# Kernel optimization log

Measured on AMD Instinct MI355X. Metric: run time of the kernel, lower is better.

The kernel has to match this reference:

```python
import jax, jax.numpy as jnp
import numpy as np

B, S, H, E, V, P = 64, 1024, 512, 512, 32000, 40


def setup_inputs() -> dict:
    key = jax.random.key(0)
    ks = jax.random.split(key, 18)
    s = 0.05  # weight scale to keep tanh/sigmoid in active range
    inp = {}
    inp["input_token"] = jax.random.randint(ks[0], (B,), 0, V, dtype=jnp.int32)
    inp["hidden"] = jax.random.normal(ks[1], (1, B, H), jnp.float32)
    inp["cell"] = jax.random.normal(ks[2], (1, B, H), jnp.float32)
    inp["encoder_outputs"] = jax.random.normal(ks[3], (B, S, H), jnp.float32)
    pos_ids = jax.random.randint(ks[4], (B, S), 0, P)
    inp["pos_onehot"] = jax.nn.one_hot(pos_ids, P, dtype=jnp.float32)
    inp["src_mask"] = jnp.zeros((B, S), dtype=bool)  # no PAD (avoids all -inf rows)
    # learned parameters (torch Linear convention: y = x @ W.T + b)
    inp["embed_table"] = jax.random.normal(ks[5], (V, E), jnp.float32) * s
    inp["W_s"] = jax.random.normal(ks[6], (H, H), jnp.float32) * s
    inp["W_h"] = jax.random.normal(ks[7], (H, H), jnp.float32) * s
    inp["V_w"] = jax.random.normal(ks[8], (H,), jnp.float32) * s
    inp["W_p"] = jax.random.normal(ks[9], (P,), jnp.float32) * s
    inp["b_p"] = jax.random.normal(ks[10], (), jnp.float32) * s
    inp["W_ih"] = jax.random.normal(ks[11], (4 * H, E + H), jnp.float32) * s
    inp["W_hh"] = jax.random.normal(ks[12], (4 * H, H), jnp.float32) * s
    inp["b_ih"] = jax.random.normal(ks[13], (4 * H,), jnp.float32) * s
    inp["b_hh"] = jax.random.normal(ks[14], (4 * H,), jnp.float32) * s
    inp["W_out"] = jax.random.normal(ks[15], (V, H), jnp.float32) * s
    inp["b_out"] = jax.random.normal(ks[16], (V,), jnp.float32) * s
    return inp


def reference(input_token, hidden, cell, encoder_outputs, pos_onehot, src_mask,
              embed_table, W_s, W_h, V_w, W_p, b_p,
              W_ih, W_hh, b_ih, b_hh, W_out, b_out):
    # embedding (dropout is identity in eval)
    emb = embed_table[input_token]                                  # (B, E)
    q = hidden[-1]                                                  # (B, H)
    # POS-gated Bahdanau attention
    qs = q @ W_s.T                                                  # (B, H)
    eh = jnp.einsum('bsh,kh->bsk', encoder_outputs, W_h)            # (B, S, H)
    energy = jnp.tanh(qs[:, None, :] + eh)                          # (B, S, H)
    scores = jnp.einsum('bsh,h->bs', energy, V_w)                   # (B, S)
    gate = jax.nn.sigmoid(pos_onehot @ W_p + b_p)                   # (B, S)
    gated = jnp.where(src_mask, jnp.float32(-1e30), scores * gate)
    attn = jax.nn.softmax(gated, axis=-1)                           # (B, S)
    context = jnp.einsum('bs,bsh->bh', attn, encoder_outputs)       # (B, H)
    # single-step, single-layer LSTM (torch gate order: i, f, g, o)
    lstm_in = jnp.concatenate([emb, context], axis=-1)              # (B, E+H)
    gates = lstm_in @ W_ih.T + hidden[0] @ W_hh.T + b_ih + b_hh     # (B, 4H)
    i, f, g, o = jnp.split(gates, 4, axis=-1)
    c1 = jax.nn.sigmoid(f) * cell[0] + jax.nn.sigmoid(i) * jnp.tanh(g)
    h1 = jax.nn.sigmoid(o) * jnp.tanh(c1)                           # (B, H)
    pred = h1 @ W_out.T + b_out                                     # (B, V)
    return (pred, h1[None], c1[None], attn)
```

## Files before the change

kernel.cpp:

```cpp
#include <hip/hip_runtime.h>

#define BB 64
#define SS 1024
#define HH 512
#define EE 512
#define VV 32000
#define PP 40

typedef __attribute__((ext_vector_type(8))) __bf16 bf16x8;
typedef __attribute__((ext_vector_type(4))) float f32x4;
typedef __attribute__((ext_vector_type(8))) unsigned short us8_t;
typedef __attribute__((ext_vector_type(4))) unsigned short us4_t;

__device__ inline float fast_tanh(float x) {
    float e = __expf(-2.0f * fabsf(x));
    float t = (1.0f - e) / (1.0f + e);
    return copysignf(t, x);
}
__device__ inline float sigmf(float x) { return 1.0f / (1.0f + __expf(-x)); }

__device__ inline unsigned int cvtpk(float lo, float hi) {
    unsigned int r;
    asm volatile("v_cvt_pk_bf16_f32 %0, %1, %2" : "=v"(r) : "v"(lo), "v"(hi));
    return r;
}
__device__ inline us8_t pack8c(float4 x, float4 y) {
    union { unsigned int u[4]; us8_t v; } r;
    r.u[0] = cvtpk(x.x, x.y); r.u[1] = cvtpk(x.z, x.w);
    r.u[2] = cvtpk(y.x, y.y); r.u[3] = cvtpk(y.z, y.w);
    return r.v;
}

__global__ __launch_bounds__(256)
void k_prep(const float* __restrict__ hidden, const float* __restrict__ Ws,
            const float* __restrict__ Wh, const float* __restrict__ pos,
            const float* __restrict__ Wp, const float* __restrict__ bp,
            unsigned short* __restrict__ wh16, float* __restrict__ qs,
            float* __restrict__ gate, float* __restrict__ ctx) {
    int blk = blockIdx.x, t = threadIdx.x;
    if (blk < 64) {
        __shared__ float hb[HH];
        int b = blk;
        for (int i = t; i < HH; i += 256) hb[i] = hidden[b * HH + i];
        __syncthreads();
        for (int n = t; n < HH; n += 256) {
            const float* wr = Ws + (size_t)n * HH;
            float acc = 0.0f;
#pragma unroll 4
            for (int k = 0; k < HH; k += 4) {
                float4 w = *(const float4*)(wr + k);
                acc += w.x * hb[k] + w.y * hb[k + 1] + w.z * hb[k + 2] + w.w * hb[k + 3];
            }
            qs[b * HH + n] = acc;
        }
    } else if (blk < 96) {
        int base = (blk - 64) * 8192 + t * 4;
#pragma unroll
        for (int j = 0; j < 8; ++j) {
            int idx = base + j * 1024;
            float4 x = *(const float4*)(Wh + idx);
            union { unsigned int u[2]; us4_t v; } r;
            r.u[0] = cvtpk(x.x, x.y); r.u[1] = cvtpk(x.z, x.w);
            *(us4_t*)(wh16 + idx) = r.v;
        }
    } else if (blk < 352) {
        int idx = (blk - 96) * 256 + t;
        const float* pr = pos + (size_t)idx * PP;
        float acc = bp[0];
#pragma unroll
        for (int j = 0; j < 10; ++j) {
            float4 x = *(const float4*)(pr + j * 4);
            acc += x.x * Wp[j * 4] + x.y * Wp[j * 4 + 1] + x.z * Wp[j * 4 + 2] + x.w * Wp[j * 4 + 3];
        }
        gate[idx] = sigmf(acc);
    } else {
        int idx = (blk - 352) * 256 + t;
#pragma unroll
        for (int j = 0; j < 16; ++j) ctx[idx * 16 + j] = 0.0f;
    }
}

__global__ __launch_bounds__(512)
void k_scores(const float* __restrict__ enc, const unsigned short* __restrict__ wh16,
              const float* __restrict__ qs, const float* __restrict__ Vw,
              float* __restrict__ part) {
    __shared__ unsigned short As[128 * 40];
    __shared__ unsigned short Bs[256 * 40];
    __shared__ float pbuf[4][128];
    int bid = blockIdx.x;
    int nh = bid >> 9, rest = bid & 511;
    int b = rest >> 3, sc = rest & 7;
    int s0 = sc * 128, n0 = nh * 256;
    int tid = threadIdx.x;
    int w = tid >> 6, lane = tid & 63;
    int wm = w >> 2, wn = w & 3;
    int l15 = lane & 15, lq = lane >> 4;

    float qv[4], vw[4];
#pragma unroll
    for (int nf = 0; nf < 4; ++nf) {
        int n = n0 + wn * 64 + nf * 16 + l15;
        qv[nf] = qs[b * HH + n];
        vw[nf] = Vw[n];
    }

    int ar = tid >> 2, akseg = tid & 3;
    const float* aSrc = enc + ((size_t)(b * SS + s0 + ar)) * HH + akseg * 8;
    int br = tid >> 1, bkseg = tid & 1;
    const unsigned short* bSrc = wh16 + (size_t)(n0 + br) * HH + bkseg * 16;
    int aOff = ar * 40 + akseg * 8;
    int bOff = br * 40 + bkseg * 16;

    int aRd[4], bRd[4];
#pragma unroll
    for (int mf = 0; mf < 4; ++mf) aRd[mf] = (wm * 64 + mf * 16 + l15) * 40 + lq * 8;
#pragma unroll
    for (int nf = 0; nf < 4; ++nf) bRd[nf] = (wn * 64 + nf * 16 + l15) * 40 + lq * 8;

    f32x4 acc[4][4];
#pragma unroll
    for (int mf = 0; mf < 4; ++mf)
#pragma unroll
        for (int nf = 0; nf < 4; ++nf) acc[mf][nf] = (f32x4){0.f, 0.f, 0.f, 0.f};

    {
        float4 a0 = *(const float4*)(aSrc);
        float4 a1 = *(const float4*)(aSrc + 4);
        us8_t b0 = *(const us8_t*)(bSrc);
        us8_t b1 = *(const us8_t*)(bSrc + 8);
        *(us8_t*)(As + aOff) = pack8c(a0, a1);
        *(us8_t*)(Bs + bOff) = b0;
        *(us8_t*)(Bs + bOff + 8) = b1;
    }
    float4 xa0 = *(const float4*)(aSrc + 32);
    float4 xa1 = *(const float4*)(aSrc + 36);
    us8_t xb0 = *(const us8_t*)(bSrc + 32);
    us8_t xb1 = *(const us8_t*)(bSrc + 40);
    asm volatile("s_waitcnt lgkmcnt(0)" ::: "memory");
    __builtin_amdgcn_s_barrier();

#pragma unroll
    for (int st = 0; st < 16; ++st) {
        float4 ya0, ya1; us8_t yb0, yb1;
        if (st < 14) {
            const float* ga = aSrc + (st + 2) * 32;
            ya0 = *(const float4*)(ga);
            ya1 = *(const float4*)(ga + 4);
            const unsigned short* gb = bSrc + (st + 2) * 32;
            yb0 = *(const us8_t*)(gb);
            yb1 = *(const us8_t*)(gb + 8);
        }
        us8_t af[4], bf[4];
#pragma unroll
        for (int mf = 0; mf < 4; ++mf) af[mf] = *(const us8_t*)(As + aRd[mf]);
#pragma unroll
        for (int nf = 0; nf < 4; ++nf) bf[nf] = *(const us8_t*)(Bs + bRd[nf]);
        asm volatile("s_waitcnt lgkmcnt(0)" ::: "memory");
        __builtin_amdgcn_s_barrier();
        if (st < 15) {
            *(us8_t*)(As + aOff) = pack8c(xa0, xa1);
            *(us8_t*)(Bs + bOff) = xb0;
            *(us8_t*)(Bs + bOff + 8) = xb1;
        }
#pragma unroll
        for (int mf = 0; mf < 4; ++mf)
#pragma unroll
            for (int nf = 0; nf < 4; ++nf)
                acc[mf][nf] = __builtin_amdgcn_mfma_f32_16x16x32_bf16(
                    __builtin_bit_cast(bf16x8, af[mf]),
                    __builtin_bit_cast(bf16x8, bf[nf]), acc[mf][nf], 0, 0, 0);
        asm volatile("s_waitcnt lgkmcnt(0)" ::: "memory");
        __builtin_amdgcn_s_barrier();
        if (st < 14) { xa0 = ya0; xa1 = ya1; xb0 = yb0; xb1 = yb1; }
    }

#pragma unroll
    for (int mf = 0; mf < 4; ++mf)
#pragma unroll
        for (int r = 0; r < 4; ++r) {
            float p = 0.0f;
#pragma unroll
            for (int nf = 0; nf < 4; ++nf)
                p += vw[nf] * fast_tanh(acc[mf][nf][r] + qv[nf]);
            p += __shfl_xor(p, 1, 64);
            p += __shfl_xor(p, 2, 64);
            p += __shfl_xor(p, 4, 64);
            p += __shfl_xor(p, 8, 64);
            if (l15 == 0) pbuf[wn][wm * 64 + mf * 16 + lq * 4 + r] = p;
        }
    __syncthreads();
    if (tid < 128) {
        part[nh * (BB * SS) + b * SS + s0 + tid] =
            pbuf[0][tid] + pbuf[1][tid] + pbuf[2][tid] + pbuf[3][tid];
    }
}

__global__ __launch_bounds__(256)
void k_context(const float* __restrict__ enc, const float* __restrict__ part,
               const float* __restrict__ gate, const unsigned char* __restrict__ mask,
               float* __restrict__ attn, float* __restrict__ ctx) {
    int b = blockIdx.x >> 4, chunk = blockIdx.x & 15;
    int s0 = chunk * 64, t = threadIdx.x;
    int w = t >> 6, ln = t & 63;
    float sum = 0.0f;
#pragma unroll
    for (int j = 0; j < 4; ++j) {
        int s = j * 256 + t;
        float raw = part[b * SS + s] + part[BB * SS + b * SS + s];
        float v = mask[b * SS + s] ? -1e30f : raw * gate[b * SS + s];
        sum += __expf(v);
    }
#pragma unroll
    for (int off = 1; off < 64; off <<= 1) sum += __shfl_xor(sum, off, 64);
    __shared__ float sl[4];
    if (ln == 0) sl[w] = sum;
    __syncthreads();
    float inv = 1.0f / (sl[0] + sl[1] + sl[2] + sl[3]);

    __shared__ float aw[64];
    if (t < 64) {
        int s = s0 + t;
        float raw = part[b * SS + s] + part[BB * SS + b * SS + s];
        float v = mask[b * SS + s] ? -1e30f : raw * gate[b * SS + s];
        float a = __expf(v) * inv;
        aw[t] = a;
        attn[b * SS + s] = a;
    }
    __syncthreads();

    const float* eb = enc + ((size_t)(b * SS + s0)) * HH + 2 * t;
    float a0 = 0.f, a1 = 0.f;
#pragma unroll 4
    for (int s = 0; s < 64; ++s) {
        float2 u = *(const float2*)(eb + (size_t)s * HH);
        a0 += aw[s] * u.x;
        a1 += aw[s] * u.y;
    }
    atomicAdd(&ctx[b * HH + 2 * t], a0);
    atomicAdd(&ctx[b * HH + 2 * t + 1], a1);
}

__global__ __launch_bounds__(256)
void k_build(const int* __restrict__ tok, const float* __restrict__ embt,
             const float* __restrict__ ctx, const float* __restrict__ hidden,
             unsigned short* __restrict__ li16, unsigned short* __restrict__ h16v) {
    int b = blockIdx.x, t = threadIdx.x;
    const float* er = embt + (size_t)tok[b] * EE;
    for (int i = 2 * t; i < HH; i += 512) {
        *(unsigned int*)(li16 + b * 1024 + i) = cvtpk(er[i], er[i + 1]);
        *(unsigned int*)(li16 + b * 1024 + 512 + i) = cvtpk(ctx[b * HH + i], ctx[b * HH + i + 1]);
        *(unsigned int*)(h16v + b * HH + i) = cvtpk(hidden[b * HH + i], hidden[b * HH + i + 1]);
    }
}

__global__ __launch_bounds__(256)
void k_gates(const unsigned short* __restrict__ li16, const unsigned short* __restrict__ h16v,
             const float* __restrict__ Wih, const float* __restrict__ Whh,
             float* __restrict__ gpart) {
    int nt = blockIdx.x >> 2, ksl = blockIdx.x & 3;
    int wave = threadIdx.x >> 6, lane = threadIdx.x & 63;
    int l15 = lane & 15, lq = lane >> 4, k0 = lq * 8;
    int n0w = nt * 128 + wave * 32;
    f32x4 acc[4][2];
#pragma unroll
    for (int mf = 0; mf < 4; ++mf)
#pragma unroll
        for (int nf = 0; nf < 2; ++nf) acc[mf][nf] = (f32x4){0.f, 0.f, 0.f, 0.f};

    for (int ks = 0; ks < 12; ++ks) {
        int kg = ksl * 384 + ks * 32;
        us8_t af[4];
        if (kg < 1024) {
#pragma unroll
            for (int mf = 0; mf < 4; ++mf)
                af[mf] = *(const us8_t*)(li16 + (mf * 16 + l15) * 1024 + kg + k0);
        } else {
#pragma unroll
            for (int mf = 0; mf < 4; ++mf)
                af[mf] = *(const us8_t*)(h16v + (mf * 16 + l15) * 512 + (kg - 1024) + k0);
        }
#pragma unroll
        for (int nf = 0; nf < 2; ++nf) {
            int n = n0w + nf * 16 + l15;
            us8_t bu;
            if (kg < 1024) {
                const float* wr = Wih + (size_t)n * 1024 + kg + k0;
                bu = pack8c(*(const float4*)wr, *(const float4*)(wr + 4));
            } else {
                const float* wr = Whh + (size_t)n * 512 + (kg - 1024) + k0;
                bu = pack8c(*(const float4*)wr, *(const float4*)(wr + 4));
            }
#pragma unroll
            for (int mf = 0; mf < 4; ++mf)
                acc[mf][nf] = __builtin_amdgcn_mfma_f32_16x16x32_bf16(
                    __builtin_bit_cast(bf16x8, af[mf]),
                    __builtin_bit_cast(bf16x8, bu), acc[mf][nf], 0, 0, 0);
        }
    }
#pragma unroll
    for (int mf = 0; mf < 4; ++mf)
#pragma unroll
        for (int nf = 0; nf < 2; ++nf)
#pragma unroll
            for (int r = 0; r < 4; ++r) {
                int row = mf * 16 + lq * 4 + r;
                int n = n0w + nf * 16 + l15;
                gpart[ksl * (BB * 2048) + row * 2048 + n] = acc[mf][nf][r];
            }
}

__global__ __launch_bounds__(512)
void k_lstm(const float* __restrict__ gpart, const float* __restrict__ bih,
            const float* __restrict__ bhh, const float* __restrict__ cell,
            float* __restrict__ oh, float* __restrict__ oc,
            unsigned short* __restrict__ h116) {
    int b = blockIdx.x, t = threadIdx.x;
    float gi = bih[t] + bhh[t];
    float gf = bih[512 + t] + bhh[512 + t];
    float gg = bih[1024 + t] + bhh[1024 + t];
    float go = bih[1536 + t] + bhh[1536 + t];
#pragma unroll
    for (int ksl = 0; ksl < 4; ++ksl) {
        const float* gp = gpart + ksl * (BB * 2048) + b * 2048;
        gi += gp[t];
        gf += gp[512 + t];
        gg += gp[1024 + t];
        go += gp[1536 + t];
    }
    float c0 = cell[b * HH + t];
    float c1 = sigmf(gf) * c0 + sigmf(gi) * fast_tanh(gg);
    float h1 = sigmf(go) * fast_tanh(c1);
    oh[b * HH + t] = h1;
    oc[b * HH + t] = c1;
    h116[b * HH + t] = (unsigned short)(cvtpk(h1, h1) & 0xffffu);
}

__global__ __launch_bounds__(512)
void k_pred(const unsigned short* __restrict__ h116, const float* __restrict__ Wout,
            const float* __restrict__ bout, float* __restrict__ pred) {
    int wave = threadIdx.x >> 6, lane = threadIdx.x & 63;
    int l15 = lane & 15, lq = lane >> 4, k0 = lq * 8;
    int n = blockIdx.x * 128 + wave * 16 + l15;
    f32x4 acc[4];
#pragma unroll
    for (int mf = 0; mf < 4; ++mf) acc[mf] = (f32x4){0.f, 0.f, 0.f, 0.f};
    const float* wr = Wout + (size_t)n * HH;
#pragma unroll 4
    for (int ks = 0; ks < 16; ++ks) {
        float4 x = *(const float4*)(wr + ks * 32 + k0);
        float4 y = *(const float4*)(wr + ks * 32 + k0 + 4);
        us8_t bu = pack8c(x, y);
#pragma unroll
        for (int mf = 0; mf < 4; ++mf) {
            us8_t au = *(const us8_t*)(h116 + (mf * 16 + l15) * 512 + ks * 32 + k0);
            acc[mf] = __builtin_amdgcn_mfma_f32_16x16x32_bf16(
                __builtin_bit_cast(bf16x8, au),
                __builtin_bit_cast(bf16x8, bu), acc[mf], 0, 0, 0);
        }
    }
    float bo = bout[n];
#pragma unroll
    for (int mf = 0; mf < 4; ++mf)
#pragma unroll
        for (int r = 0; r < 4; ++r) {
            int row = mf * 16 + lq * 4 + r;
            pred[(size_t)row * VV + n] = acc[mf][r] + bo;
        }
}

extern "C" void kernel_launch(void* const* d_in, const int* in_sizes, int n_in,
                              void* d_out, int out_size, void* d_ws, size_t ws_size,
                              hipStream_t stream) {
    const int* tok = (const int*)d_in[0];
    const float* hidden = (const float*)d_in[1];
    const float* cell = (const float*)d_in[2];
    const float* enc = (const float*)d_in[3];
    const float* pos = (const float*)d_in[4];
    const unsigned char* mask = (const unsigned char*)d_in[5];
    const float* embt = (const float*)d_in[6];
    const float* Ws = (const float*)d_in[7];
    const float* Wh = (const float*)d_in[8];
    const float* Vw = (const float*)d_in[9];
    const float* Wp = (const float*)d_in[10];
    const float* bp = (const float*)d_in[11];
    const float* Wih = (const float*)d_in[12];
    const float* Whh = (const float*)d_in[13];
    const float* bih = (const float*)d_in[14];
    const float* bhh = (const float*)d_in[15];
    const float* Wout = (const float*)d_in[16];
    const float* bout = (const float*)d_in[17];

    float* out = (float*)d_out;
    float* pred = out;
    float* out_h = out + 2048000;
    float* out_c = out + 2080768;
    float* attn = out + 2113536;

    char* wsb = (char*)d_ws;
    unsigned short* wh16 = (unsigned short*)(wsb);
    float* qs = (float*)(wsb + (512 << 10));
    float* gate = (float*)(wsb + (640 << 10));
    float* part = (float*)(wsb + (896 << 10));
    float* ctx = (float*)(wsb + (1408 << 10));
    unsigned short* li16 = (unsigned short*)(wsb + (1536 << 10));
    unsigned short* h16v = (unsigned short*)(wsb + (1664 << 10));
    float* gpart = (float*)(wsb + (1728 << 10));
    unsigned short* h116 = (unsigned short*)(wsb + (3776 << 10));

    hipLaunchKernelGGL(k_prep, dim3(360), dim3(256), 0, stream,
                       hidden, Ws, Wh, pos, Wp, bp, wh16, qs, gate, ctx);
    hipLaunchKernelGGL(k_scores, dim3(1024), dim3(512), 0, stream,
                       enc, wh16, qs, Vw, part);
    hipLaunchKernelGGL(k_context, dim3(1024), dim3(256), 0, stream,
                       enc, part, gate, mask, attn, ctx);
    hipLaunchKernelGGL(k_build, dim3(64), dim3(256), 0, stream,
                       tok, embt, ctx, hidden, li16, h16v);
    hipLaunchKernelGGL(k_gates, dim3(64), dim3(256), 0, stream, li16, h16v, Wih, Whh, gpart);
    hipLaunchKernelGGL(k_lstm, dim3(64), dim3(512), 0, stream,
                       gpart, bih, bhh, cell, out_h, out_c, h116);
    hipLaunchKernelGGL(k_pred, dim3(250), dim3(512), 0, stream, h116, Wout, bout, pred);
}
```

Measured before the change: 175.8 us.

## Double-buffer LDS tiles in scores GEMM and drop a barrier per k-step

The scores GEMM kernel now keeps two LDS buffers for the A (encoder, bf16) and B (W_h) tiles. Each k-step reads the current buffer while writing the next one, which removes one of the two barriers per iteration. The global prefetch now reuses the same registers instead of a separate staging set. The LDS row stride also drops from 40 to 36 elements. That roughly doubles LDS use and gives 72-byte rows, so 16-byte vector LDS accesses are no longer 16-byte aligned and may be split or bank-conflict differently.

New measurement: 272.6 us. 1.55x slower.

```diff
diff --git a/kernel.cpp b/kernel.cpp
--- a/kernel.cpp
+++ b/kernel.cpp
@@ -30,6 +30,8 @@
     r.u[2] = cvtpk(y.x, y.y); r.u[3] = cvtpk(y.z, y.w);
     return r.v;
 }
+
+#define LSTRIDE 36
 
 __global__ __launch_bounds__(256)
 void k_prep(const float* __restrict__ hidden, const float* __restrict__ Ws,
@@ -84,8 +86,8 @@
 void k_scores(const float* __restrict__ enc, const unsigned short* __restrict__ wh16,
               const float* __restrict__ qs, const float* __restrict__ Vw,
               float* __restrict__ part) {
-    __shared__ unsigned short As[128 * 40];
-    __shared__ unsigned short Bs[256 * 40];
+    __shared__ unsigned short As[2][128 * LSTRIDE];
+    __shared__ unsigned short Bs[2][256 * LSTRIDE];
     __shared__ float pbuf[4][128];
     int bid = blockIdx.x;
     int nh = bid >> 9, rest = bid & 511;
@@ -108,14 +110,14 @@
     const float* aSrc = enc + ((size_t)(b * SS + s0 + ar)) * HH + akseg * 8;
     int br = tid >> 1, bkseg = tid & 1;
     const unsigned short* bSrc = wh16 + (size_t)(n0 + br) * HH + bkseg * 16;
-    int aOff = ar * 40 + akseg * 8;
-    int bOff = br * 40 + bkseg * 16;
+    int aOff = ar * LSTRIDE + akseg * 8;
+    int bOff = br * LSTRIDE + bkseg * 16;
 
     int aRd[4], bRd[4];
 #pragma unroll
-    for (int mf = 0; mf < 4; ++mf) aRd[mf] = (wm * 64 + mf * 16 + l15) * 40 + lq * 8;
-#pragma unroll
-    for (int nf = 0; nf < 4; ++nf) bRd[nf] = (wn * 64 + nf * 16 + l15) * 40 + lq * 8;
+    for (int mf = 0; mf < 4; ++mf) aRd[mf] = (wm * 64 + mf * 16 + l15) * LSTRIDE + lq * 8;
+#pragma unroll
+    for (int nf = 0; nf < 4; ++nf) bRd[nf] = (wn * 64 + nf * 16 + l15) * LSTRIDE + lq * 8;
 
     f32x4 acc[4][4];
 #pragma unroll
@@ -128,9 +130,9 @@
         float4 a1 = *(const float4*)(aSrc + 4);
         us8_t b0 = *(const us8_t*)(bSrc);
         us8_t b1 = *(const us8_t*)(bSrc + 8);
-        *(us8_t*)(As + aOff) = pack8c(a0, a1);
-        *(us8_t*)(Bs + bOff) = b0;
-        *(us8_t*)(Bs + bOff + 8) = b1;
+        *(us8_t*)(&As[0][aOff]) = pack8c(a0, a1);
+        *(us8_t*)(&Bs[0][bOff]) = b0;
+        *(us8_t*)(&Bs[0][bOff + 8]) = b1;
     }
     float4 xa0 = *(const float4*)(aSrc + 32);
     float4 xa1 = *(const float4*)(aSrc + 36);
@@ -141,27 +143,31 @@
 
 #pragma unroll
     for (int st = 0; st < 16; ++st) {
-        float4 ya0, ya1; us8_t yb0, yb1;
+        const unsigned short* Ac = As[st & 1];
+        const unsigned short* Bc = Bs[st & 1];
+        unsigned short* An = (unsigned short*)As[(st + 1) & 1];
+        unsigned short* Bn = (unsigned short*)Bs[(st + 1) & 1];
+
+        us8_t af[4], bf[4];
+#pragma unroll
+        for (int mf = 0; mf < 4; ++mf) af[mf] = *(const us8_t*)(Ac + aRd[mf]);
+#pragma unroll
+        for (int nf = 0; nf < 4; ++nf) bf[nf] = *(const us8_t*)(Bc + bRd[nf]);
+
+        if (st < 15) {
+            *(us8_t*)(An + aOff) = pack8c(xa0, xa1);
+            *(us8_t*)(Bn + bOff) = xb0;
+            *(us8_t*)(Bn + bOff + 8) = xb1;
+        }
         if (st < 14) {
             const float* ga = aSrc + (st + 2) * 32;
-            ya0 = *(const float4*)(ga);
-            ya1 = *(const float4*)(ga + 4);
             const unsigned short* gb = bSrc + (st + 2) * 32;
-            yb0 = *(const us8_t*)(gb);
-            yb1 = *(const us8_t*)(gb + 8);
-        }
-        us8_t af[4], bf[4];
-#pragma unroll
-        for (int mf = 0; mf < 4; ++mf) af[mf] = *(const us8_t*)(As + aRd[mf]);
-#pragma unroll
-        for (int nf = 0; nf < 4; ++nf) bf[nf] = *(const us8_t*)(Bs + bRd[nf]);
-        asm volatile("s_waitcnt lgkmcnt(0)" ::: "memory");
-        __builtin_amdgcn_s_barrier();
-        if (st < 15) {
-            *(us8_t*)(As + aOff) = pack8c(xa0, xa1);
-            *(us8_t*)(Bs + bOff) = xb0;
-            *(us8_t*)(Bs + bOff + 8) = xb1;
-        }
+            xa0 = *(const float4*)(ga);
+            xa1 = *(const float4*)(ga + 4);
+            xb0 = *(const us8_t*)(gb);
+            xb1 = *(const us8_t*)(gb + 8);
+        }
+
 #pragma unroll
         for (int mf = 0; mf < 4; ++mf)
 #pragma unroll
@@ -169,9 +175,9 @@
                 acc[mf][nf] = __builtin_amdgcn_mfma_f32_16x16x32_bf16(
                     __builtin_bit_cast(bf16x8, af[mf]),
                     __builtin_bit_cast(bf16x8, bf[nf]), acc[mf][nf], 0, 0, 0);
+
         asm volatile("s_waitcnt lgkmcnt(0)" ::: "memory");
         __builtin_amdgcn_s_barrier();
-        if (st < 14) { xa0 = ya0; xa1 = ya1; xb0 = yb0; xb1 = yb1; }
     }
 
 #pragma unroll
```

## Use direct global-to-LDS loads with double buffering and swizzle in scores GEMM

Applied to the files above, without the earlier changes.

Rewrites the k_scores main loop to stream fp32 encoder tiles and bf16 W_h tiles straight into double-buffered LDS via global_load_lds, with XOR-swizzled layouts to avoid bank conflicts. The fp32-to-bf16 conversion moves from the store side to after the LDS read. The goal is to drop the register staging and one barrier per step, and to overlap global loads with MFMA work. The cost is a larger LDS footprint, since A is now kept as fp32 and double-buffered, which may lower occupancy. Correctness also relies on vmcnt counting and the swizzle mapping being right.

Result: faster. 171.4 us, median of 3 (-2.5%).

```diff
diff --git a/kernel.cpp b/kernel.cpp
--- a/kernel.cpp
+++ b/kernel.cpp
@@ -21,7 +21,7 @@
 
 __device__ inline unsigned int cvtpk(float lo, float hi) {
     unsigned int r;
-    asm volatile("v_cvt_pk_bf16_f32 %0, %1, %2" : "=v"(r) : "v"(lo), "v"(hi));
+    asm("v_cvt_pk_bf16_f32 %0, %1, %2" : "=v"(r) : "v"(lo), "v"(hi));
     return r;
 }
 __device__ inline us8_t pack8c(float4 x, float4 y) {
@@ -30,13 +30,25 @@
     r.u[2] = cvtpk(y.x, y.y); r.u[3] = cvtpk(y.z, y.w);
     return r.v;
 }
+__device__ inline us8_t pack8v(f32x4 a, f32x4 b) {
+    union { unsigned int u[4]; us8_t v; } r;
+    r.u[0] = cvtpk(a[0], a[1]); r.u[1] = cvtpk(a[2], a[3]);
+    r.u[2] = cvtpk(b[0], b[1]); r.u[3] = cvtpk(b[2], b[3]);
+    return r.v;
+}
+
+typedef __attribute__((address_space(1))) const unsigned char gas_t;
+typedef __attribute__((address_space(3))) unsigned char las_t;
+__device__ inline void gload16(const void* g, void* l) {
+    __builtin_amdgcn_global_load_lds((gas_t*)g, (las_t*)l, 16, 0, 0);
+}
 
 __global__ __launch_bounds__(256)
-void k_prep(const float* __restrict__ hidden, const float* __restrict__ Ws,
-            const float* __restrict__ Wh, const float* __restrict__ pos,
-            const float* __restrict__ Wp, const float* __restrict__ bp,
-            unsigned short* __restrict__ wh16, float* __restrict__ qs,
-            float* __restrict__ gate, float* __restrict__ ctx) {
+void k_pre(const float* __restrict__ hidden, const float* __restrict__ Ws,
+           const float* __restrict__ Wh, const float* __restrict__ pos,
+           const float* __restrict__ Wp, const float* __restrict__ bp,
+           unsigned short* __restrict__ wh16, float* __restrict__ qs,
+           float* __restrict__ gate, float* __restrict__ ctx) {
     int blk = blockIdx.x, t = threadIdx.x;
     if (blk < 64) {
         __shared__ float hb[HH];
@@ -81,11 +93,12 @@
 }
 
 __global__ __launch_bounds__(512)
-void k_scores(const float* __restrict__ enc, const unsigned short* __restrict__ wh16,
+void k_scores(const float* __restrict__ enc,
+              const unsigned short* __restrict__ wh16,
               const float* __restrict__ qs, const float* __restrict__ Vw,
               float* __restrict__ part) {
-    __shared__ unsigned short As[128 * 40];
-    __shared__ unsigned short Bs[256 * 40];
+    __shared__ float As[2][4096];
+    __shared__ unsigned short Bs[2][8192];
     __shared__ float pbuf[4][128];
     int bid = blockIdx.x;
     int nh = bid >> 9, rest = bid & 511;
@@ -104,18 +117,27 @@
         vw[nf] = Vw[n];
     }
 
-    int ar = tid >> 2, akseg = tid & 3;
-    const float* aSrc = enc + ((size_t)(b * SS + s0 + ar)) * HH + akseg * 8;
-    int br = tid >> 1, bkseg = tid & 1;
-    const unsigned short* bSrc = wh16 + (size_t)(n0 + br) * HH + bkseg * 16;
-    int aOff = ar * 40 + akseg * 8;
-    int bOff = br * 40 + bkseg * 16;
-
-    int aRd[4], bRd[4];
-#pragma unroll
-    for (int mf = 0; mf < 4; ++mf) aRd[mf] = (wm * 64 + mf * 16 + l15) * 40 + lq * 8;
-#pragma unroll
-    for (int nf = 0; nf < 4; ++nf) bRd[nf] = (wn * 64 + nf * 16 + l15) * 40 + lq * 8;
+    unsigned int colbA = (unsigned int)(((lane & 7) * 16) ^ ((lane >> 3) << 4));
+    unsigned int colbB = (unsigned int)(((lane & 3) * 16) ^ (((lane >> 3) & 3) << 4));
+    const char* gA0 = (const char*)(enc + (size_t)(b * SS + s0) * HH);
+    const char* gB0 = (const char*)(wh16 + (size_t)n0 * HH);
+    int aRowS = w * 8 + (lane >> 3);
+    int bRowS = w * 16 + (lane >> 2);
+    int ldsOff = w * 1024 + lane * 16;
+
+    int aRowB[4], akey[4], bRowB[4], bkey[4];
+#pragma unroll
+    for (int mf = 0; mf < 4; ++mf) {
+        int r = wm * 64 + mf * 16 + l15;
+        aRowB[mf] = r * 128;
+        akey[mf] = (r & 7) << 4;
+    }
+#pragma unroll
+    for (int nf = 0; nf < 4; ++nf) {
+        int r = wn * 64 + nf * 16 + l15;
+        bRowB[nf] = r * 64;
+        bkey[nf] = ((r >> 1) & 3) << 4;
+    }
 
     f32x4 acc[4][4];
 #pragma unroll
@@ -123,56 +145,57 @@
 #pragma unroll
         for (int nf = 0; nf < 4; ++nf) acc[mf][nf] = (f32x4){0.f, 0.f, 0.f, 0.f};
 
-    {
-        float4 a0 = *(const float4*)(aSrc);
-        float4 a1 = *(const float4*)(aSrc + 4);
-        us8_t b0 = *(const us8_t*)(bSrc);
-        us8_t b1 = *(const us8_t*)(bSrc + 8);
-        *(us8_t*)(As + aOff) = pack8c(a0, a1);
-        *(us8_t*)(Bs + bOff) = b0;
-        *(us8_t*)(Bs + bOff + 8) = b1;
-    }
-    float4 xa0 = *(const float4*)(aSrc + 32);
-    float4 xa1 = *(const float4*)(aSrc + 36);
-    us8_t xb0 = *(const us8_t*)(bSrc + 32);
-    us8_t xb1 = *(const us8_t*)(bSrc + 40);
-    asm volatile("s_waitcnt lgkmcnt(0)" ::: "memory");
-    __builtin_amdgcn_s_barrier();
-
-#pragma unroll
-    for (int st = 0; st < 16; ++st) {
-        float4 ya0, ya1; us8_t yb0, yb1;
-        if (st < 14) {
-            const float* ga = aSrc + (st + 2) * 32;
-            ya0 = *(const float4*)(ga);
-            ya1 = *(const float4*)(ga + 4);
-            const unsigned short* gb = bSrc + (st + 2) * 32;
-            yb0 = *(const us8_t*)(gb);
-            yb1 = *(const us8_t*)(gb + 8);
-        }
-        us8_t af[4], bf[4];
-#pragma unroll
-        for (int mf = 0; mf < 4; ++mf) af[mf] = *(const us8_t*)(As + aRd[mf]);
-#pragma unroll
-        for (int nf = 0; nf < 4; ++nf) bf[nf] = *(const us8_t*)(Bs + bRd[nf]);
-        asm volatile("s_waitcnt lgkmcnt(0)" ::: "memory");
+#define STAGE(BUF, KT)                                                          \
+    {                                                                           \
+        _Pragma("unroll")                                                       \
+        for (int p = 0; p < 2; ++p) {                                           \
+            const char* ga = gA0 + (size_t)(p * 64 + aRowS) * 2048 +            \
+                             (KT) * 128 + colbA;                                \
+            gload16(ga, (char*)As[BUF] + p * 8192 + ldsOff);                    \
+            const char* gb = gB0 + (size_t)(p * 128 + bRowS) * 1024 +           \
+                             (KT) * 64 + colbB;                                 \
+            gload16(gb, (char*)Bs[BUF] + p * 8192 + ldsOff);                    \
+        }                                                                       \
+    }
+
+#define COMPUTE(BUF)                                                            \
+    {                                                                           \
+        us8_t af[4], bf[4];                                                     \
+        _Pragma("unroll")                                                       \
+        for (int mf = 0; mf < 4; ++mf) {                                        \
+            const char* pa = (const char*)As[BUF] + aRowB[mf];                  \
+            f32x4 a0 = *(const f32x4*)(pa + ((lq * 32) ^ akey[mf]));            \
+            f32x4 a1 = *(const f32x4*)(pa + ((lq * 32 + 16) ^ akey[mf]));       \
+            af[mf] = pack8v(a0, a1);                                            \
+        }                                                                       \
+        _Pragma("unroll")                                                       \
+        for (int nf = 0; nf < 4; ++nf)                                          \
+            bf[nf] = *(const us8_t*)((const char*)Bs[BUF] + bRowB[nf] +         \
+                                     ((lq * 16) ^ bkey[nf]));                   \
+        _Pragma("unroll")                                                       \
+        for (int mf = 0; mf < 4; ++mf)                                          \
+            _Pragma("unroll")                                                   \
+            for (int nf = 0; nf < 4; ++nf)                                      \
+                acc[mf][nf] = __builtin_amdgcn_mfma_f32_16x16x32_bf16(          \
+                    __builtin_bit_cast(bf16x8, af[mf]),                         \
+                    __builtin_bit_cast(bf16x8, bf[nf]), acc[mf][nf], 0, 0, 0);  \
+    }
+
+    STAGE(0, 0);
+#pragma unroll
+    for (int kt = 0; kt < 16; ++kt) {
+        if (kt < 15) {
+            STAGE((kt + 1) & 1, kt + 1);
+            asm volatile("s_waitcnt vmcnt(4)" ::: "memory");
+        } else {
+            asm volatile("s_waitcnt vmcnt(0)" ::: "memory");
+        }
         __builtin_amdgcn_s_barrier();
-        if (st < 15) {
-            *(us8_t*)(As + aOff) = pack8c(xa0, xa1);
-            *(us8_t*)(Bs + bOff) = xb0;
-            *(us8_t*)(Bs + bOff + 8) = xb1;
-        }
-#pragma unroll
-        for (int mf = 0; mf < 4; ++mf)
-#pragma unroll
-            for (int nf = 0; nf < 4; ++nf)
-                acc[mf][nf] = __builtin_amdgcn_mfma_f32_16x16x32_bf16(
-                    __builtin_bit_cast(bf16x8, af[mf]),
-                    __builtin_bit_cast(bf16x8, bf[nf]), acc[mf][nf], 0, 0, 0);
-        asm volatile("s_waitcnt lgkmcnt(0)" ::: "memory");
+        COMPUTE(kt & 1);
         __builtin_amdgcn_s_barrier();
-        if (st < 14) { xa0 = ya0; xa1 = ya1; xb0 = yb0; xb1 = yb1; }
-    }
+    }
+#undef STAGE
+#undef COMPUTE
 
 #pragma unroll
     for (int mf = 0; mf < 4; ++mf)
@@ -407,7 +430,7 @@
     float* gpart = (float*)(wsb + (1728 << 10));
     unsigned short* h116 = (unsigned short*)(wsb + (3776 << 10));
 
-    hipLaunchKernelGGL(k_prep, dim3(360), dim3(256), 0, stream,
+    hipLaunchKernelGGL(k_pre, dim3(360), dim3(256), 0, stream,
                        hidden, Ws, Wh, pos, Wp, bp, wh16, qs, gate, ctx);
     hipLaunchKernelGGL(k_scores, dim3(1024), dim3(512), 0, stream,
                        enc, wh16, qs, Vw, part);
```
